# Kernel tuning notes

Measured on AMD Instinct MI355X. Metric: run time of the kernel, lower is better.

Reference implementation:

```python
import jax, jax.numpy as jnp
import numpy as np

BS, SEQ, HID = 2, 2048, 1024
HEADS, BLOCK = 16, 64
HEAD_DIM = HID // HEADS


def setup_inputs() -> dict:
    key = jax.random.key(0)
    ks = jax.random.split(key, 5)
    s = 1.0 / np.sqrt(HID)
    return {
        "hidden_states": jax.random.normal(ks[0], (BS, SEQ, HID), jnp.float32),
        "Wq": jax.random.normal(ks[1], (HID, HID), jnp.float32) * s,
        "bq": jnp.zeros((HID,), jnp.float32),
        "Wk": jax.random.normal(ks[2], (HID, HID), jnp.float32) * s,
        "bk": jnp.zeros((HID,), jnp.float32),
        "Wv": jax.random.normal(ks[3], (HID, HID), jnp.float32) * s,
        "bv": jnp.zeros((HID,), jnp.float32),
        "Wo": jax.random.normal(ks[4], (HID, HID), jnp.float32) * s,
        "bo": jnp.zeros((HID,), jnp.float32),
    }


def reference(hidden_states, Wq, bq, Wk, bk, Wv, bv, Wo, bo):
    b, s, _ = hidden_states.shape
    # torch Linear: y = x @ W.T + b
    q = (hidden_states @ Wq.T + bq).reshape(b, s, HEADS, HEAD_DIM)
    k = (hidden_states @ Wk.T + bk).reshape(b, s, HEADS, HEAD_DIM)
    v = (hidden_states @ Wv.T + bv).reshape(b, s, HEADS, HEAD_DIM)
    scale = 1.0 / np.sqrt(HEAD_DIM).astype(np.float32)
    scores = jnp.einsum("bqhd,bkhd->bhqk", q, k) * scale  # [B,H,S,S]
    # block-level causal mask: kv block index <= query block index
    blk = jnp.arange(s) // BLOCK
    mask = blk[None, :] <= blk[:, None]  # [S,S]
    scores = jnp.where(mask[None, None], scores, jnp.finfo(scores.dtype).min)
    attn = jax.nn.softmax(scores, axis=-1)
    out = jnp.einsum("bhqk,bkhd->bqhd", attn, v).reshape(b, s, HID)
    return out @ Wo.T + bo
```

## Files before the change

### kernel.cpp

```cpp
#include <hip/hip_runtime.h>

#define BS 2
#define SEQ 2048
#define HID 1024
#define HEADS 16
#define HDIM 64
#define MTOT (BS * SEQ)

typedef __bf16 bf16x8 __attribute__((ext_vector_type(8)));
typedef float floatx4 __attribute__((ext_vector_type(4)));
typedef short short8 __attribute__((ext_vector_type(8)));
typedef unsigned short u16x4 __attribute__((ext_vector_type(4)));
typedef unsigned int u32x2 __attribute__((ext_vector_type(2)));

__device__ __forceinline__ floatx4 mfma16x16x32bf16(short8 a, short8 b, floatx4 c) {
    return __builtin_amdgcn_mfma_f32_16x16x32_bf16(
        __builtin_bit_cast(bf16x8, a), __builtin_bit_cast(bf16x8, b), c, 0, 0, 0);
}

__device__ __forceinline__ unsigned short f2bf(float f) {
    unsigned int u = __builtin_bit_cast(unsigned int, f);
    u += 0x7fffu + ((u >> 16) & 1u);
    return (unsigned short)(u >> 16);
}

#define GLOAD_LDS16(gsrc, ldst)                                                   \
    __builtin_amdgcn_global_load_lds(                                             \
        (const __attribute__((address_space(1))) void*)(gsrc),                    \
        (__attribute__((address_space(3))) void*)(ldst), 16, 0, 0)

__global__ __launch_bounds__(256) void cvt5(
    const float* __restrict__ X, const float* __restrict__ Wq,
    const float* __restrict__ Wk, const float* __restrict__ Wv,
    const float* __restrict__ Wo, unsigned short* __restrict__ dst)
{
    const int y = blockIdx.y;
    const float* src = (y == 0) ? X : (y == 1) ? Wq : (y == 2) ? Wk : (y == 3) ? Wv : Wo;
    const size_t base = (y == 0) ? 0 : (size_t)(4u << 20) + (size_t)(y - 1) * (1u << 20);
    const int n4 = (y == 0) ? (1 << 20) : (1 << 18);
    const float scale = (y == 1) ? 0.125f : 1.0f;
    int i = blockIdx.x * 256 + threadIdx.x;
    if (i >= n4) return;
    floatx4 v = *(const floatx4*)(src + (size_t)i * 4);
    v *= scale;
    unsigned int p0 = (unsigned int)f2bf(v[0]) | ((unsigned int)f2bf(v[1]) << 16);
    unsigned int p1 = (unsigned int)f2bf(v[2]) | ((unsigned int)f2bf(v[3]) << 16);
    u32x2 pk = {p0, p1};
    *(u32x2*)(dst + base + (size_t)i * 4) = pk;
}

__global__ __launch_bounds__(256) void gemm_qkv(
    const unsigned short* __restrict__ X,
    const unsigned short* __restrict__ W0, const unsigned short* __restrict__ W1,
    const unsigned short* __restrict__ W2,
    const float* __restrict__ B0, const float* __restrict__ B1,
    const float* __restrict__ B2,
    unsigned short* __restrict__ out_bf)
{
    __shared__ __align__(16) unsigned short sA[64 * 32];
    __shared__ __align__(16) unsigned short sB[3][128 * 32];

    const int tid  = threadIdx.x;
    const int m0   = blockIdx.x * 64;
    const int n0   = blockIdx.y * 128;
    const int lane = tid & 63, w = tid >> 6;
    const int l16  = lane & 15, grp = lane >> 4;
    const int wm   = w & 1, wn = w >> 1;

    const unsigned short* Wz[3] = {W0, W1, W2};

    floatx4 acc[3][2][4];
#pragma unroll
    for (int z = 0; z < 3; ++z)
#pragma unroll
        for (int i = 0; i < 2; ++i)
#pragma unroll
            for (int j = 0; j < 4; ++j) acc[z][i][j] = (floatx4){0.f, 0.f, 0.f, 0.f};

    auto stage = [&](int kb) {
        const int kcol = kb * 32;
        {
            int row = tid >> 2, c8 = (tid & 3) * 8;
            GLOAD_LDS16(X + (size_t)(m0 + row) * HID + kcol + c8, &sA[tid * 8]);
        }
#pragma unroll
        for (int i = 0; i < 6; ++i) {
            int g2 = tid + i * 256;
            int z = g2 >> 9, g3 = g2 & 511;
            int row = g3 >> 2, c8 = (g3 & 3) * 8;
            GLOAD_LDS16(Wz[z] + (size_t)(n0 + row) * HID + kcol + c8, &sB[z][g3 * 8]);
        }
    };

    stage(0);
    for (int kb = 0; kb < 32; ++kb) {
        __syncthreads();
        short8 af[2], bfr[3][4];
#pragma unroll
        for (int t = 0; t < 2; ++t)
            af[t] = *(const short8*)&sA[(wm * 32 + t * 16 + l16) * 32 + grp * 8];
#pragma unroll
        for (int z = 0; z < 3; ++z)
#pragma unroll
            for (int t = 0; t < 4; ++t)
                bfr[z][t] = *(const short8*)&sB[z][(wn * 64 + t * 16 + l16) * 32 + grp * 8];
        __syncthreads();
        if (kb + 1 < 32) stage(kb + 1);
#pragma unroll
        for (int mt = 0; mt < 2; ++mt)
#pragma unroll
            for (int nt = 0; nt < 4; ++nt) {
                acc[0][mt][nt] = mfma16x16x32bf16(bfr[0][nt], af[mt], acc[0][mt][nt]);
                acc[1][mt][nt] = mfma16x16x32bf16(bfr[1][nt], af[mt], acc[1][mt][nt]);
                acc[2][mt][nt] = mfma16x16x32bf16(af[mt], bfr[2][nt], acc[2][mt][nt]);
            }
    }

    const int hidx = (n0 + wn * 64) >> 6;
    {
#pragma unroll
        for (int nt = 0; nt < 4; ++nt) {
            int dbase = nt * 16 + grp * 4;
            floatx4 b4 = *(const floatx4*)&B0[n0 + wn * 64 + dbase];
            b4 *= 0.125f;
#pragma unroll
            for (int mt = 0; mt < 2; ++mt) {
                int m = m0 + wm * 32 + mt * 16 + l16;
                int bidx = m >> 11, s = m & (SEQ - 1);
                u16x4 pk;
#pragma unroll
                for (int r = 0; r < 4; ++r) pk[r] = f2bf(acc[0][mt][nt][r] + b4[r]);
                *(u16x4*)&out_bf[
                    ((((size_t)bidx * HEADS + hidx) * SEQ + s) * HDIM + dbase)] = pk;
            }
        }
    }
    {
        const size_t outz = (size_t)MTOT * HID;
        const int bidx = m0 >> 11;
        const int kvb  = (m0 & (SEQ - 1)) >> 6;
        const size_t hbase = outz + ((size_t)bidx * HEADS + hidx) * SEQ * HDIM;
        const int grpf = grp >> 1, j0 = (grp & 1) * 4;
#pragma unroll
        for (int nt = 0; nt < 4; ++nt) {
            floatx4 b4 = *(const floatx4*)&B1[n0 + wn * 64 + nt * 16 + grp * 4];
#pragma unroll
            for (int mt = 0; mt < 2; ++mt) {
                u16x4 pk;
#pragma unroll
                for (int r = 0; r < 4; ++r) pk[r] = f2bf(acc[1][mt][nt][r] + b4[r]);
                size_t F = hbase
                    + (size_t)((((kvb * 4 + (wm * 2 + mt)) * 2 + (nt >> 1)) * 512)
                    + ((((nt & 1) * 2 + grpf) * 16 + l16) * 8) + j0);
                *(u16x4*)&out_bf[F] = pk;
            }
        }
    }
    {
        const size_t outz = (size_t)2 * ((size_t)MTOT * HID);
        const int bidx = m0 >> 11;
        const int kvb  = (m0 & (SEQ - 1)) >> 6;
        const size_t hbase = outz + ((size_t)bidx * HEADS + hidx) * SEQ * HDIM;
        const int j0 = (grp & 1) * 4;
#pragma unroll
        for (int nt = 0; nt < 4; ++nt) {
            float bias = B2[n0 + wn * 64 + nt * 16 + l16];
#pragma unroll
            for (int mt = 0; mt < 2; ++mt) {
                u16x4 pk;
#pragma unroll
                for (int r = 0; r < 4; ++r) pk[r] = f2bf(acc[2][mt][nt][r] + bias);
                size_t F = hbase + (size_t)((((kvb * 4 + nt) * 2 + wm) * 512)
                    + (((mt * 2 + (grp >> 1)) * 16 + l16) * 8) + j0);
                *(u16x4*)&out_bf[F] = pk;
            }
        }
    }
}

template <int BM, int BN>
__global__ __launch_bounds__(256) void gemm_out(
    const unsigned short* __restrict__ X, const unsigned short* __restrict__ W,
    const float* __restrict__ Bb, float* __restrict__ out_f)
{
    constexpr int MT = BM / 32, NT = BN / 32;
    constexpr int NCH = (BM + BN) * 4;
    __shared__ __align__(16) unsigned short sA[BM * 32];
    __shared__ __align__(16) unsigned short sB[BN * 32];

    const int tid  = threadIdx.x;
    const int m0   = blockIdx.x * BM;
    const int n0   = blockIdx.y * BN;
    const int lane = tid & 63, w = tid >> 6;
    const int l16  = lane & 15, grp = lane >> 4;
    const int wm   = w & 1, wn = w >> 1;

    floatx4 acc[MT][NT];
#pragma unroll
    for (int i = 0; i < MT; ++i)
#pragma unroll
        for (int j = 0; j < NT; ++j) acc[i][j] = (floatx4){0.f, 0.f, 0.f, 0.f};

    auto stage = [&](int kb) {
        const int kcol = kb * 32;
#pragma unroll
        for (int i = 0; i < NCH / 256; ++i) {
            int g = tid + i * 256;
            if (g < BM * 4) {
                int row = g >> 2, c8 = (g & 3) * 8;
                GLOAD_LDS16(X + (size_t)(m0 + row) * HID + kcol + c8, &sA[g * 8]);
            } else {
                int g2 = g - BM * 4;
                int row = g2 >> 2, c8 = (g2 & 3) * 8;
                GLOAD_LDS16(W + (size_t)(n0 + row) * HID + kcol + c8, &sB[g2 * 8]);
            }
        }
    };

    stage(0);
    for (int kb = 0; kb < 32; ++kb) {
        __syncthreads();
        short8 af[MT], bfr[NT];
#pragma unroll
        for (int t = 0; t < MT; ++t)
            af[t] = *(const short8*)&sA[(wm * (BM / 2) + t * 16 + l16) * 32 + grp * 8];
#pragma unroll
        for (int t = 0; t < NT; ++t)
            bfr[t] = *(const short8*)&sB[(wn * (BN / 2) + t * 16 + l16) * 32 + grp * 8];
        __syncthreads();
        if (kb + 1 < 32) stage(kb + 1);
#pragma unroll
        for (int mt = 0; mt < MT; ++mt)
#pragma unroll
            for (int nt = 0; nt < NT; ++nt)
                acc[mt][nt] = mfma16x16x32bf16(af[mt], bfr[nt], acc[mt][nt]);
    }

#pragma unroll
    for (int nt = 0; nt < NT; ++nt) {
        int n = n0 + wn * (BN / 2) + nt * 16 + l16;
        float bias = Bb[n];
#pragma unroll
        for (int mt = 0; mt < MT; ++mt)
#pragma unroll
            for (int r = 0; r < 4; ++r) {
                int m = m0 + wm * (BM / 2) + mt * 16 + grp * 4 + r;
                out_f[(size_t)m * HID + n] = acc[mt][nt][r] + bias;
            }
    }
}

__global__ __launch_bounds__(64) void attn_kernel(
    const unsigned short* __restrict__ Qw, const unsigned short* __restrict__ Kf,
    const unsigned short* __restrict__ Vf, unsigned short* __restrict__ X2)
{
    __shared__ __align__(16) unsigned short Ps[16][72];

    const int id = blockIdx.x;
    const int xcd = id & 7, k = id >> 3;
    const int bh  = (k >> 6) * 8 + xcd;
    const int slot = k & 63;
    const int pairj = slot >> 2;
    const int quarter = slot & 3;
    const int b = bh >> 4, h = bh & 15;

    const int lane = threadIdx.x & 63;
    const int l16  = lane & 15, grp = lane >> 4;

    const size_t head = ((size_t)b * HEADS + h) * (size_t)SEQ * HDIM;
    const unsigned short* Kh = Kf + head;
    const unsigned short* Vh = Vf + head;

    short8 ka[4][2], kbuf[4][2], vf[4][2];

    auto loadK = [&](short8 (&kf)[4][2], int kb) {
#pragma unroll
        for (int nt = 0; nt < 4; ++nt)
#pragma unroll
            for (int ks = 0; ks < 2; ++ks)
                kf[nt][ks] = *(const short8*)(Kh +
                    (size_t)(((kb * 4 + nt) * 2 + ks) * 512) + lane * 8);
    };

#pragma unroll 1
    for (int phase = 0; phase < 2; ++phase) {
        const int qblk = phase ? (31 - pairj) : pairj;
        const int nkb  = qblk + 1;
        const int q0   = qblk * 64 + quarter * 16;

        short8 qf[2];
#pragma unroll
        for (int ks = 0; ks < 2; ++ks)
            qf[ks] = *(const short8*)(Qw + head +
                (size_t)(q0 + l16) * HDIM + ks * 32 + grp * 8);

        floatx4 o[4];
#pragma unroll
        for (int i = 0; i < 4; ++i) o[i] = (floatx4){0.f, 0.f, 0.f, 0.f};
        float mi = -1e30f, li = 0.f;

        auto process = [&](short8 (&kfc)[4][2], short8 (&kfn)[4][2], int kb) {
            {
#pragma unroll
                for (int nt = 0; nt < 4; ++nt)
#pragma unroll
                    for (int ks = 0; ks < 2; ++ks)
                        vf[nt][ks] = *(const short8*)(Vh +
                            (size_t)(((kb * 4 + nt) * 2 + ks) * 512) + lane * 8);
            }
            floatx4 sv[4];
#pragma unroll
            for (int nt = 0; nt < 4; ++nt) {
                floatx4 zz = (floatx4){0.f, 0.f, 0.f, 0.f};
                zz = mfma16x16x32bf16(kfc[nt][0], qf[0], zz);
                zz = mfma16x16x32bf16(kfc[nt][1], qf[1], zz);
                sv[nt] = zz;
            }
            if (kb + 1 < nkb) loadK(kfn, kb + 1);

            float m01 = fmaxf(fmaxf(sv[0][0], sv[0][1]), fmaxf(sv[0][2], sv[0][3]));
            float m23 = fmaxf(fmaxf(sv[1][0], sv[1][1]), fmaxf(sv[1][2], sv[1][3]));
            float m45 = fmaxf(fmaxf(sv[2][0], sv[2][1]), fmaxf(sv[2][2], sv[2][3]));
            float m67 = fmaxf(fmaxf(sv[3][0], sv[3][1]), fmaxf(sv[3][2], sv[3][3]));
            float mx = fmaxf(fmaxf(m01, m23), fmaxf(m45, m67));
            mx = fmaxf(mx, __shfl_xor(mx, 16));
            mx = fmaxf(mx, __shfl_xor(mx, 32));
            float mn = fmaxf(mi, mx);
            float alpha = __expf(mi - mn);
            mi = mn;
            float rs = 0.f;
#pragma unroll
            for (int nt = 0; nt < 4; ++nt) {
                floatx4 p;
#pragma unroll
                for (int r = 0; r < 4; ++r) p[r] = __expf(sv[nt][r] - mn);
                sv[nt] = p;
                rs += (p[0] + p[1]) + (p[2] + p[3]);
            }
            rs += __shfl_xor(rs, 16);
            rs += __shfl_xor(rs, 32);
            li = li * alpha + rs;

#pragma unroll
            for (int nt = 0; nt < 4; ++nt) {
                u16x4 pk;
#pragma unroll
                for (int r = 0; r < 4; ++r) pk[r] = f2bf(sv[nt][r]);
                *(u16x4*)&Ps[l16][nt * 16 + grp * 4] = pk;
            }
#pragma unroll
            for (int dt = 0; dt < 4; ++dt) o[dt] *= alpha;

            short8 pf0 = *(const short8*)&Ps[l16][grp * 8];
            short8 pf1 = *(const short8*)&Ps[l16][32 + grp * 8];
#pragma unroll
            for (int dt = 0; dt < 4; ++dt) {
                o[dt] = mfma16x16x32bf16(vf[dt][0], pf0, o[dt]);
                o[dt] = mfma16x16x32bf16(vf[dt][1], pf1, o[dt]);
            }
        };

        loadK(ka, 0);
        int kb = 0;
        while (true) {
            process(ka, kbuf, kb);
            if (++kb >= nkb) break;
            process(kbuf, ka, kb);
            if (++kb >= nkb) break;
        }

        float inv = 1.0f / li;
        int srow = q0 + l16;
#pragma unroll
        for (int dt = 0; dt < 4; ++dt) {
            u16x4 pk;
#pragma unroll
            for (int r = 0; r < 4; ++r) pk[r] = f2bf(o[dt][r] * inv);
            *(u16x4*)&X2[((size_t)b * SEQ + srow) * HID +
                         h * HDIM + dt * 16 + grp * 4] = pk;
        }
    }
}

extern "C" void kernel_launch(void* const* d_in, const int* in_sizes, int n_in,
                              void* d_out, int out_size, void* d_ws, size_t ws_size,
                              hipStream_t stream) {
    int iX, iWq, ibq, iWk, ibk, iWv, ibv, iWo, ibo;
    if (in_sizes[0] == MTOT * HID) {
        iX = 0; iWq = 1; ibq = 2; iWk = 3; ibk = 4; iWv = 5; ibv = 6; iWo = 7; ibo = 8;
    } else {
        iWk = 0; iWo = 1; iWq = 2; iWv = 3; ibk = 4; ibo = 5; ibq = 6; ibv = 7; iX = 8;
    }
    const float* X  = (const float*)d_in[iX];
    const float* Wq = (const float*)d_in[iWq];
    const float* bq = (const float*)d_in[ibq];
    const float* Wk = (const float*)d_in[iWk];
    const float* bk = (const float*)d_in[ibk];
    const float* Wv = (const float*)d_in[iWv];
    const float* bv = (const float*)d_in[ibv];
    const float* Wo = (const float*)d_in[iWo];
    const float* bo = (const float*)d_in[ibo];
    float* out = (float*)d_out;

    unsigned short* ws = (unsigned short*)d_ws;
    const size_t T = (size_t)MTOT * HID;
    unsigned short* qw  = ws;
    unsigned short* kfr = ws + T;
    unsigned short* vfr = ws + 2 * T;
    unsigned short* x2  = ws + 3 * T;
    unsigned short* Xb  = ws + 4 * T;
    unsigned short* Wqb = Xb + T;
    unsigned short* Wkb = Wqb + (size_t)HID * HID;
    unsigned short* Wvb = Wkb + (size_t)HID * HID;
    unsigned short* Wob = Wvb + (size_t)HID * HID;

    cvt5<<<dim3(4096, 5), 256, 0, stream>>>(X, Wq, Wk, Wv, Wo, Xb);
    gemm_qkv<<<dim3(64, 8), 256, 0, stream>>>(
        Xb, Wqb, Wkb, Wvb, bq, bk, bv, qw);
    attn_kernel<<<dim3(2048), 64, 0, stream>>>(qw, kfr, vfr, x2);
    gemm_out<64, 128><<<dim3(64, 8), 256, 0, stream>>>(x2, Wob, bo, out);
}
```

Baseline: 190.2 us.

## Use exp2 softmax with lazy rescale, packed bf16 converts, and one q-block per workgroup

Folds log2(e) into the Q scale so softmax uses hardware exp2, and skips the running-max rescale unless the max grows by more than a threshold. All bf16 conversions switch to the packed v_cvt_pk_bf16_f32 instruction. The attention grid doubles so each workgroup handles a single query block, heaviest first, instead of a balanced pair. MFMA sections are wrapped in s_setprio. The lazy rescale keeps exps bounded but relies on the threshold, and dropping the pairing may change load balance.

```diff
diff --git a/kernel.cpp b/kernel.cpp
--- a/kernel.cpp
+++ b/kernel.cpp
@@ -7,6 +7,8 @@
 #define HDIM 64
 #define MTOT (BS * SEQ)
 
+#define QSCALE 0.18033688f
+
 typedef __bf16 bf16x8 __attribute__((ext_vector_type(8)));
 typedef float floatx4 __attribute__((ext_vector_type(4)));
 typedef short short8 __attribute__((ext_vector_type(8)));
@@ -22,6 +24,20 @@
     unsigned int u = __builtin_bit_cast(unsigned int, f);
     u += 0x7fffu + ((u >> 16) & 1u);
     return (unsigned short)(u >> 16);
+}
+
+__device__ __forceinline__ unsigned int cvt_pk_bf16(float lo, float hi) {
+    unsigned int r;
+    asm("v_cvt_pk_bf16_f32 %0, %1, %2" : "=v"(r) : "v"(lo), "v"(hi));
+    return r;
+}
+
+__device__ __forceinline__ float fast_exp2(float x) {
+#if __has_builtin(__builtin_amdgcn_exp2f)
+    return __builtin_amdgcn_exp2f(x);
+#else
+    return __expf(x * 0.6931471805599453f);
+#endif
 }
 
 #define GLOAD_LDS16(gsrc, ldst)                                                   \
@@ -38,7 +54,7 @@
     const float* src = (y == 0) ? X : (y == 1) ? Wq : (y == 2) ? Wk : (y == 3) ? Wv : Wo;
     const size_t base = (y == 0) ? 0 : (size_t)(4u << 20) + (size_t)(y - 1) * (1u << 20);
     const int n4 = (y == 0) ? (1 << 20) : (1 << 18);
-    const float scale = (y == 1) ? 0.125f : 1.0f;
+    const float scale = (y == 1) ? QSCALE : 1.0f;
     int i = blockIdx.x * 256 + threadIdx.x;
     if (i >= n4) return;
     floatx4 v = *(const floatx4*)(src + (size_t)i * 4);
@@ -122,15 +138,15 @@
         for (int nt = 0; nt < 4; ++nt) {
             int dbase = nt * 16 + grp * 4;
             floatx4 b4 = *(const floatx4*)&B0[n0 + wn * 64 + dbase];
-            b4 *= 0.125f;
+            b4 *= QSCALE;
 #pragma unroll
             for (int mt = 0; mt < 2; ++mt) {
                 int m = m0 + wm * 32 + mt * 16 + l16;
                 int bidx = m >> 11, s = m & (SEQ - 1);
-                u16x4 pk;
-#pragma unroll
-                for (int r = 0; r < 4; ++r) pk[r] = f2bf(acc[0][mt][nt][r] + b4[r]);
-                *(u16x4*)&out_bf[
+                u32x2 pk;
+                pk[0] = cvt_pk_bf16(acc[0][mt][nt][0] + b4[0], acc[0][mt][nt][1] + b4[1]);
+                pk[1] = cvt_pk_bf16(acc[0][mt][nt][2] + b4[2], acc[0][mt][nt][3] + b4[3]);
+                *(u32x2*)&out_bf[
                     ((((size_t)bidx * HEADS + hidx) * SEQ + s) * HDIM + dbase)] = pk;
             }
         }
@@ -146,13 +162,13 @@
             floatx4 b4 = *(const floatx4*)&B1[n0 + wn * 64 + nt * 16 + grp * 4];
 #pragma unroll
             for (int mt = 0; mt < 2; ++mt) {
-                u16x4 pk;
-#pragma unroll
-                for (int r = 0; r < 4; ++r) pk[r] = f2bf(acc[1][mt][nt][r] + b4[r]);
+                u32x2 pk;
+                pk[0] = cvt_pk_bf16(acc[1][mt][nt][0] + b4[0], acc[1][mt][nt][1] + b4[1]);
+                pk[1] = cvt_pk_bf16(acc[1][mt][nt][2] + b4[2], acc[1][mt][nt][3] + b4[3]);
                 size_t F = hbase
                     + (size_t)((((kvb * 4 + (wm * 2 + mt)) * 2 + (nt >> 1)) * 512)
                     + ((((nt & 1) * 2 + grpf) * 16 + l16) * 8) + j0);
-                *(u16x4*)&out_bf[F] = pk;
+                *(u32x2*)&out_bf[F] = pk;
             }
         }
     }
@@ -167,12 +183,12 @@
             float bias = B2[n0 + wn * 64 + nt * 16 + l16];
 #pragma unroll
             for (int mt = 0; mt < 2; ++mt) {
-                u16x4 pk;
-#pragma unroll
-                for (int r = 0; r < 4; ++r) pk[r] = f2bf(acc[2][mt][nt][r] + bias);
+                u32x2 pk;
+                pk[0] = cvt_pk_bf16(acc[2][mt][nt][0] + bias, acc[2][mt][nt][1] + bias);
+                pk[1] = cvt_pk_bf16(acc[2][mt][nt][2] + bias, acc[2][mt][nt][3] + bias);
                 size_t F = hbase + (size_t)((((kvb * 4 + nt) * 2 + wm) * 512)
                     + (((mt * 2 + (grp >> 1)) * 16 + l16) * 8) + j0);
-                *(u16x4*)&out_bf[F] = pk;
+                *(u32x2*)&out_bf[F] = pk;
             }
         }
     }
@@ -258,9 +274,9 @@
 
     const int id = blockIdx.x;
     const int xcd = id & 7, k = id >> 3;
-    const int bh  = (k >> 6) * 8 + xcd;
-    const int slot = k & 63;
-    const int pairj = slot >> 2;
+    const int bh  = (k >> 7) * 8 + xcd;
+    const int slot = k & 127;
+    const int qblk = 31 - (slot >> 2);
     const int quarter = slot & 3;
     const int b = bh >> 4, h = bh & 15;
 
@@ -282,103 +298,106 @@
                     (size_t)(((kb * 4 + nt) * 2 + ks) * 512) + lane * 8);
     };
 
-#pragma unroll 1
-    for (int phase = 0; phase < 2; ++phase) {
-        const int qblk = phase ? (31 - pairj) : pairj;
-        const int nkb  = qblk + 1;
-        const int q0   = qblk * 64 + quarter * 16;
-
-        short8 qf[2];
-#pragma unroll
-        for (int ks = 0; ks < 2; ++ks)
-            qf[ks] = *(const short8*)(Qw + head +
-                (size_t)(q0 + l16) * HDIM + ks * 32 + grp * 8);
-
-        floatx4 o[4];
-#pragma unroll
-        for (int i = 0; i < 4; ++i) o[i] = (floatx4){0.f, 0.f, 0.f, 0.f};
-        float mi = -1e30f, li = 0.f;
-
-        auto process = [&](short8 (&kfc)[4][2], short8 (&kfn)[4][2], int kb) {
-            {
-#pragma unroll
-                for (int nt = 0; nt < 4; ++nt)
-#pragma unroll
-                    for (int ks = 0; ks < 2; ++ks)
-                        vf[nt][ks] = *(const short8*)(Vh +
-                            (size_t)(((kb * 4 + nt) * 2 + ks) * 512) + lane * 8);
-            }
-            floatx4 sv[4];
-#pragma unroll
-            for (int nt = 0; nt < 4; ++nt) {
-                floatx4 zz = (floatx4){0.f, 0.f, 0.f, 0.f};
-                zz = mfma16x16x32bf16(kfc[nt][0], qf[0], zz);
-                zz = mfma16x16x32bf16(kfc[nt][1], qf[1], zz);
-                sv[nt] = zz;
-            }
-            if (kb + 1 < nkb) loadK(kfn, kb + 1);
-
-            float m01 = fmaxf(fmaxf(sv[0][0], sv[0][1]), fmaxf(sv[0][2], sv[0][3]));
-            float m23 = fmaxf(fmaxf(sv[1][0], sv[1][1]), fmaxf(sv[1][2], sv[1][3]));
-            float m45 = fmaxf(fmaxf(sv[2][0], sv[2][1]), fmaxf(sv[2][2], sv[2][3]));
-            float m67 = fmaxf(fmaxf(sv[3][0], sv[3][1]), fmaxf(sv[3][2], sv[3][3]));
-            float mx = fmaxf(fmaxf(m01, m23), fmaxf(m45, m67));
-            mx = fmaxf(mx, __shfl_xor(mx, 16));
-            mx = fmaxf(mx, __shfl_xor(mx, 32));
+    const int nkb = qblk + 1;
+    const int q0  = qblk * 64 + quarter * 16;
+
+    short8 qf[2];
+#pragma unroll
+    for (int ks = 0; ks < 2; ++ks)
+        qf[ks] = *(const short8*)(Qw + head +
+            (size_t)(q0 + l16) * HDIM + ks * 32 + grp * 8);
+
+    floatx4 o[4];
+#pragma unroll
+    for (int i = 0; i < 4; ++i) o[i] = (floatx4){0.f, 0.f, 0.f, 0.f};
+    float mi = -1e30f, li = 0.f;
+
+    auto process = [&](short8 (&kfc)[4][2], short8 (&kfn)[4][2], int kb) {
+        {
+#pragma unroll
+            for (int nt = 0; nt < 4; ++nt)
+#pragma unroll
+                for (int ks = 0; ks < 2; ++ks)
+                    vf[nt][ks] = *(const short8*)(Vh +
+                        (size_t)(((kb * 4 + nt) * 2 + ks) * 512) + lane * 8);
+        }
+        floatx4 sv[4];
+        __builtin_amdgcn_s_setprio(1);
+#pragma unroll
+        for (int nt = 0; nt < 4; ++nt) {
+            floatx4 zz = (floatx4){0.f, 0.f, 0.f, 0.f};
+            zz = mfma16x16x32bf16(kfc[nt][0], qf[0], zz);
+            zz = mfma16x16x32bf16(kfc[nt][1], qf[1], zz);
+            sv[nt] = zz;
+        }
+        __builtin_amdgcn_s_setprio(0);
+        if (kb + 1 < nkb) loadK(kfn, kb + 1);
+
+        float m01 = fmaxf(fmaxf(sv[0][0], sv[0][1]), fmaxf(sv[0][2], sv[0][3]));
+        float m23 = fmaxf(fmaxf(sv[1][0], sv[1][1]), fmaxf(sv[1][2], sv[1][3]));
+        float m45 = fmaxf(fmaxf(sv[2][0], sv[2][1]), fmaxf(sv[2][2], sv[2][3]));
+        float m67 = fmaxf(fmaxf(sv[3][0], sv[3][1]), fmaxf(sv[3][2], sv[3][3]));
+        float mx = fmaxf(fmaxf(m01, m23), fmaxf(m45, m67));
+        mx = fmaxf(mx, __shfl_xor(mx, 16));
+        mx = fmaxf(mx, __shfl_xor(mx, 32));
+        if (!__all(mx - mi <= 8.f)) {
             float mn = fmaxf(mi, mx);
-            float alpha = __expf(mi - mn);
+            float alpha = fast_exp2(mi - mn);
             mi = mn;
-            float rs = 0.f;
-#pragma unroll
-            for (int nt = 0; nt < 4; ++nt) {
-                floatx4 p;
-#pragma unroll
-                for (int r = 0; r < 4; ++r) p[r] = __expf(sv[nt][r] - mn);
-                sv[nt] = p;
-                rs += (p[0] + p[1]) + (p[2] + p[3]);
-            }
-            rs += __shfl_xor(rs, 16);
-            rs += __shfl_xor(rs, 32);
-            li = li * alpha + rs;
-
-#pragma unroll
-            for (int nt = 0; nt < 4; ++nt) {
-                u16x4 pk;
-#pragma unroll
-                for (int r = 0; r < 4; ++r) pk[r] = f2bf(sv[nt][r]);
-                *(u16x4*)&Ps[l16][nt * 16 + grp * 4] = pk;
-            }
+            li *= alpha;
 #pragma unroll
             for (int dt = 0; dt < 4; ++dt) o[dt] *= alpha;
-
-            short8 pf0 = *(const short8*)&Ps[l16][grp * 8];
-            short8 pf1 = *(const short8*)&Ps[l16][32 + grp * 8];
-#pragma unroll
-            for (int dt = 0; dt < 4; ++dt) {
-                o[dt] = mfma16x16x32bf16(vf[dt][0], pf0, o[dt]);
-                o[dt] = mfma16x16x32bf16(vf[dt][1], pf1, o[dt]);
-            }
-        };
-
-        loadK(ka, 0);
-        int kb = 0;
-        while (true) {
-            process(ka, kbuf, kb);
-            if (++kb >= nkb) break;
-            process(kbuf, ka, kb);
-            if (++kb >= nkb) break;
-        }
-
-        float inv = 1.0f / li;
-        int srow = q0 + l16;
+        }
+        float rs = 0.f;
+#pragma unroll
+        for (int nt = 0; nt < 4; ++nt) {
+            floatx4 p;
+#pragma unroll
+            for (int r = 0; r < 4; ++r) p[r] = fast_exp2(sv[nt][r] - mi);
+            sv[nt] = p;
+            rs += (p[0] + p[1]) + (p[2] + p[3]);
+        }
+        rs += __shfl_xor(rs, 16);
+        rs += __shfl_xor(rs, 32);
+        li += rs;
+
+#pragma unroll
+        for (int nt = 0; nt < 4; ++nt) {
+            u32x2 pk;
+            pk[0] = cvt_pk_bf16(sv[nt][0], sv[nt][1]);
+            pk[1] = cvt_pk_bf16(sv[nt][2], sv[nt][3]);
+            *(u32x2*)&Ps[l16][nt * 16 + grp * 4] = pk;
+        }
+
+        short8 pf0 = *(const short8*)&Ps[l16][grp * 8];
+        short8 pf1 = *(const short8*)&Ps[l16][32 + grp * 8];
+        __builtin_amdgcn_s_setprio(1);
 #pragma unroll
         for (int dt = 0; dt < 4; ++dt) {
-            u16x4 pk;
-#pragma unroll
-            for (int r = 0; r < 4; ++r) pk[r] = f2bf(o[dt][r] * inv);
-            *(u16x4*)&X2[((size_t)b * SEQ + srow) * HID +
-                         h * HDIM + dt * 16 + grp * 4] = pk;
-        }
+            o[dt] = mfma16x16x32bf16(vf[dt][0], pf0, o[dt]);
+            o[dt] = mfma16x16x32bf16(vf[dt][1], pf1, o[dt]);
+        }
+        __builtin_amdgcn_s_setprio(0);
+    };
+
+    loadK(ka, 0);
+    int kb = 0;
+    while (true) {
+        process(ka, kbuf, kb);
+        if (++kb >= nkb) break;
+        process(kbuf, ka, kb);
+        if (++kb >= nkb) break;
+    }
+
+    float inv = 1.0f / li;
+    int srow = q0 + l16;
+#pragma unroll
+    for (int dt = 0; dt < 4; ++dt) {
+        u32x2 pk;
+        pk[0] = cvt_pk_bf16(o[dt][0] * inv, o[dt][1] * inv);
+        pk[1] = cvt_pk_bf16(o[dt][2] * inv, o[dt][3] * inv);
+        *(u32x2*)&X2[((size_t)b * SEQ + srow) * HID +
+                     h * HDIM + dt * 16 + grp * 4] = pk;
     }
 }
 
@@ -417,6 +436,6 @@
     cvt5<<<dim3(4096, 5), 256, 0, stream>>>(X, Wq, Wk, Wv, Wo, Xb);
     gemm_qkv<<<dim3(64, 8), 256, 0, stream>>>(
         Xb, Wqb, Wkb, Wvb, bq, bk, bv, qw);
-    attn_kernel<<<dim3(2048), 64, 0, stream>>>(qw, kfr, vfr, x2);
+    attn_kernel<<<dim3(4096), 64, 0, stream>>>(qw, kfr, vfr, x2);
     gemm_out<64, 128><<<dim3(64, 8), 256, 0, stream>>>(x2, Wob, bo, out);
 }
```

After: 197.7 us. 4.0% more time.
